# Kernel optimization log

Hardware: AMD Instinct MI355X
Metric: run time of the kernel (lower is better)

Reference implementation:

```python
import jax, jax.numpy as jnp
import numpy as np
from jax import lax

N, C_IN, C_OUT, W_DIM, RES = 16, 512, 512, 512, 64
K = 3                       # conv kernel (non-torgb)
UP, DOWN = 2, 2             # filtered_lrelu up/down factors
TAPS = 6 * UP               # 12-tap FIR filters (filter_size * factor)
FS = 128.0                  # tmp_sampling_rate = 2 * 64
CUTOFF, WIDTH = 8.0, 48.0   # cutoff Hz, transition width = 2*half_width
SLOPE, GAIN, CLAMP = 0.2, float(np.sqrt(2)), 256.0

# filtered_lrelu padding (StyleGAN3 formula); symmetric since square images
_pt = (RES - 1) * DOWN + 1 - (RES + K - 1) * UP + 2 * TAPS - 2
PX0 = PY0 = (_pt + UP) // 2   # = 9
PX1 = PY1 = _pt - PX0         # = 8


def design_lowpass_filter(numtaps, cutoff, width, fs):
    # scipy.signal.firwin with Kaiser window (width given), normalized to unit DC gain
    nyq = 0.5 * fs
    wn = width / nyq
    a = 2.285 * (numtaps - 1) * np.pi * wn + 7.95  # kaiser_atten
    if a > 50:
        beta = 0.1102 * (a - 8.7)
    elif a > 21:
        beta = 0.5842 * (a - 21) ** 0.4 + 0.07886 * (a - 21)
    else:
        beta = 0.0
    win = np.kaiser(numtaps, beta)
    m = np.arange(numtaps) - (numtaps - 1) / 2
    c = cutoff / nyq
    h = c * np.sinc(c * m) * win
    return (h / h.sum()).astype(np.float32)


def setup_inputs() -> dict:
    key = jax.random.key(0)
    ks = jax.random.split(key, 5)
    f = jnp.asarray(design_lowpass_filter(TAPS, CUTOFF, WIDTH, FS))
    return {
        "x": jax.random.normal(ks[0], (N, C_IN, RES, RES), jnp.float32),
        "w": jax.random.normal(ks[1], (N, W_DIM), jnp.float32),
        "affine_weight": jax.random.normal(ks[2], (C_IN, W_DIM), jnp.float32),
        "affine_bias": jnp.ones((C_IN,), jnp.float32),  # bias_init=1
        "conv_weight": jax.random.normal(ks[3], (C_OUT, C_IN, K, K), jnp.float32),
        "conv_bias": 0.1 * jax.random.normal(ks[4], (C_OUT,), jnp.float32),
        "up_filter": f,
        "down_filter": f,
    }


def _upfirdn2d_sep(x, f, up, down, pads, gain):
    # Separable upfirdn2d: zero-insert upsample, pad, FIR conv, strided downsample.
    # lhs_dilation gives (H-1)*up+1 samples; the up-1 trailing zeros of the torch
    # reference contribute nothing, so fold them into the high-side padding.
    px0, px1, py0, py1 = pads
    n, c, h, w = x.shape
    x = x.reshape(n * c, 1, h, w)
    x = lax.conv_general_dilated(x, f[None, None, :, None], (down, 1),
                                 [(py0, py1 + up - 1), (0, 0)], lhs_dilation=(up, 1),
                                 dimension_numbers=('NCHW', 'OIHW', 'NCHW'))
    x = lax.conv_general_dilated(x, f[None, None, None, :], (1, down),
                                 [(0, 0), (px0, px1 + up - 1)], lhs_dilation=(1, up),
                                 dimension_numbers=('NCHW', 'OIHW', 'NCHW'))
    return (x * gain).reshape(n, c, x.shape[2], x.shape[3])


def reference(x, w, affine_weight, affine_bias, conv_weight, conv_bias, up_filter, down_filter):
    # FullyConnectedLayer: weight_gain = 1/sqrt(w_dim)
    styles = w @ affine_weight.T * (1.0 / np.sqrt(W_DIM)) + affine_bias  # [N, C_IN]
    input_gain = 1.0  # magnitude_ema buffer == 1 -> rsqrt == 1

    # modulated_conv2d with demodulation (pre-normalize weight and styles)
    wt = conv_weight * lax.rsqrt(jnp.mean(conv_weight ** 2, axis=(1, 2, 3), keepdims=True))
    s = styles * lax.rsqrt(jnp.mean(styles ** 2))
    wk = wt[None] * s[:, None, :, None, None]             # [N, O, I, k, k]
    d = lax.rsqrt(jnp.sum(wk ** 2, axis=(2, 3, 4)) + 1e-8)  # [N, O]
    wk = wk * d[:, :, None, None, None] * input_gain

    def conv_one(xi, wi):  # xi [C,H,W], wi [O,I,k,k]; padding = kernel-1 = 2
        return lax.conv_general_dilated(xi[None], wi, (1, 1), [(K - 1, K - 1)] * 2,
                                        dimension_numbers=('NCHW', 'OIHW', 'NCHW'))[0]

    y = jax.vmap(conv_one)(x, wk)                         # [N, O, 66, 66]

    # filtered_lrelu: bias -> FIR upsample (gain=up^2) -> lrelu*sqrt(2)+clamp -> FIR downsample
    y = y + conv_bias[None, :, None, None]
    y = _upfirdn2d_sep(y, up_filter, UP, 1, (PX0, PX1, PY0, PY1), float(UP * UP))
    y = jnp.where(y >= 0, y, SLOPE * y) * GAIN
    y = jnp.clip(y, -CLAMP, CLAMP)
    y = _upfirdn2d_sep(y, down_filter, 1, DOWN, (0, 0, 0, 0), 1.0)
    return y  # [N, O, 64, 64]
```

## Files before the change

### kernel.cpp

```cpp
#include <hip/hip_runtime.h>
#include <hip/hip_bf16.h>

typedef __attribute__((ext_vector_type(8))) short bf16x8;
typedef __attribute__((ext_vector_type(4))) float f32x4;
typedef unsigned int u32;
typedef const __attribute__((address_space(1))) u32 glb_u32;
typedef __attribute__((address_space(3))) u32 lds_u32;

#define NB 16
#define CI 512
#define CO 512
#define PC 66
#define PADD 68
#define NCOLS (NB*PC*PC)

#define WS_STYLES 0ul
#define WS_SNORM  32768ul
#define WS_D      33024ul
#define WS_W2     65792ul
#define WS_AT     1114368ul
#define WS_XS     5832960ul
#define WS_CONV   81592576ul

__global__ void k_styles(const float* __restrict__ w, const float* __restrict__ aw,
                         const float* __restrict__ ab, float* __restrict__ styles) {
  int idx = blockIdx.x * 256 + threadIdx.x;
  int n = idx >> 9, i = idx & 511;
  const float* wr = w + n * 512;
  const float* ar = aw + i * 512;
  float s = 0.f;
  for (int j = 0; j < 512; ++j) s += wr[j] * ar[j];
  styles[idx] = s * 0.04419417382415922f + ab[i];
}

__global__ void k_snorm(const float* __restrict__ styles, float* __restrict__ snorm) {
  __shared__ float red[256];
  float s = 0.f;
  for (int e = threadIdx.x; e < 8192; e += 256) { float v = styles[e]; s += v * v; }
  red[threadIdx.x] = s;
  __syncthreads();
  for (int st = 128; st > 0; st >>= 1) {
    if (threadIdx.x < st) red[threadIdx.x] += red[threadIdx.x + st];
    __syncthreads();
  }
  if (threadIdx.x == 0) snorm[0] = rsqrtf(red[0] / 8192.f);
}

__global__ void k_wprep(const float* __restrict__ cw, __hip_bfloat16* __restrict__ At,
                        float* __restrict__ W2) {
  int o = blockIdx.x;
  const float* base = cw + o * 4608;
  __shared__ float red[256];
  __shared__ float wnorm_s;
  float s = 0.f;
  for (int e = threadIdx.x; e < 4608; e += 256) { float v = base[e]; s += v * v; }
  red[threadIdx.x] = s;
  __syncthreads();
  for (int st = 128; st > 0; st >>= 1) {
    if (threadIdx.x < st) red[threadIdx.x] += red[threadIdx.x + st];
    __syncthreads();
  }
  if (threadIdx.x == 0) wnorm_s = rsqrtf(red[0] / 4608.f);
  __syncthreads();
  float wn = wnorm_s;
  for (int i = threadIdx.x; i < 512; i += 256) {
    const float* e9 = cw + (o * 512 + i) * 9;
    float w2 = 0.f;
    int ic = i >> 5, ik = i & 31;
#pragma unroll
    for (int rs = 0; rs < 9; ++rs) {
      float wv = e9[rs] * wn;
      w2 += wv * wv;
      At[((ic * 9 + rs) * 512 + o) * 32 + ik] = __float2bfloat16(wv);
    }
    W2[o * 512 + i] = w2;
  }
}

__global__ void k_dcalc(const float* __restrict__ W2, const float* __restrict__ styles,
                        const float* __restrict__ snorm, float* __restrict__ d) {
  int idx = blockIdx.x * 256 + threadIdx.x;
  int n = idx >> 9, o = idx & 511;
  const float* w2r = W2 + o * 512;
  const float* sr = styles + n * 512;
  float sum = 0.f;
  for (int i = 0; i < 512; ++i) { float sv = sr[i]; sum += w2r[i] * sv * sv; }
  float sn = snorm[0];
  d[idx] = rsqrtf(sn * sn * sum + 1e-8f);
}

__global__ void k_zero_border(uint4* __restrict__ p) {
  int e = blockIdx.x * 256 + threadIdx.x;
  if (e >= 16 * 528 * 64) return;
  int chunk = e & 63;
  int rest = e >> 6;
  int n = rest / 528;
  int pos = rest - n * 528;
  int row, col;
  if (pos < 272) {
    int r = pos / 68;
    row = (r < 2) ? r : r + 64;
    col = pos - r * 68;
  } else {
    int q = pos - 272;
    row = 2 + (q >> 2);
    int cs = q & 3;
    col = (cs < 2) ? cs : cs + 64;
  }
  uint4 z = {0u, 0u, 0u, 0u};
  p[(n * 4624 + row * 68 + col) * 64 + chunk] = z;
}

__global__ void k_scale_tr(const float* __restrict__ x, const float* __restrict__ styles,
                           const float* __restrict__ snorm, __hip_bfloat16* __restrict__ xs) {
  const int i0 = blockIdx.x * 64;
  const int p = blockIdx.y;
  const int n = blockIdx.z;
  __shared__ float tile[64][65];
  const float sn = snorm[0];
  const int lo = threadIdx.x & 63;
  const int hi = threadIdx.x >> 6;
#pragma unroll 4
  for (int rep = 0; rep < 16; ++rep) {
    int ii = hi + rep * 4;
    float sc = styles[n * 512 + i0 + ii] * sn;
    tile[ii][lo] = x[((n * 512 + i0 + ii) * 64 + p) * 64 + lo] * sc;
  }
  __syncthreads();
  const int obase = (n * 4624 + (p + 2) * 68 + 2) * 512 + i0;
#pragma unroll 4
  for (int rep = 0; rep < 16; ++rep) {
    int q = hi + rep * 4;
    xs[obase + q * 512 + lo] = __float2bfloat16(tile[lo][q]);
  }
}

__device__ __forceinline__ int colbase_of(int c) {
  c = c < (NCOLS - 1) ? c : (NCOLS - 1);
  int n = (int)((unsigned)c / 4356u);
  int rem = c - n * 4356;
  int p = (int)((unsigned)rem / 66u);
  int q = rem - p * 66;
  return (n * 4624 + p * 68 + q) * 512;
}


#define GLD(G, L) __builtin_amdgcn_global_load_lds((glb_u32*)(G), (lds_u32*)(L), 16, 0, 0)
#define STAGE(KT2, KOFF2, CUR) do { \
    const char* _ga = AgA + (size_t)(KT2) * 32768; \
    char* _l = smem + (CUR) + sdst; \
    GLD(_ga, _l); \
    GLD(_ga + 4096, _l + 4096); \
    GLD(_ga + 8192, _l + 8192); \
    GLD(_ga + 12288, _l + 12288); \
    GLD(xsB0 + (KOFF2), _l + 16384); \
    GLD(xsB1 + (KOFF2), _l + 20480); } while (0)
#define BARR() __builtin_amdgcn_s_barrier()
#define LGKM() asm volatile("s_waitcnt lgkmcnt(0)" ::: "memory")
#define VMC6() asm volatile("s_waitcnt vmcnt(6)" ::: "memory")
#define VMC0() asm volatile("s_waitcnt vmcnt(0)" ::: "memory")

__global__ __launch_bounds__(256, 2) void k_gemm(
    const __hip_bfloat16* __restrict__ At, const __hip_bfloat16* __restrict__ xs,
    const float* __restrict__ dnorm, const float* __restrict__ cbias,
    __hip_bfloat16* __restrict__ cvt) {
  __shared__ __align__(16) char smem[49152];
  const int tid = threadIdx.x;

  const int bid = blockIdx.x;
  const int xcd = bid & 7, sidx = bid >> 3;
  const int wgid = (xcd < 2 ? xcd * 137 : 274 + (xcd - 2) * 136) + sidx;
  const int o0 = (wgid & 1) * 256;
  const int c0 = (wgid >> 1) * 128;

  const int lane = tid & 63, wave = tid >> 6;
  const int wr = wave >> 1, wc = wave & 1;
  const int r16 = lane & 15, sx = lane >> 4;
  const int poff = (r16 >> 1) * 128 + (((((r16 & 1) << 2) | sx)) ^ (r16 >> 1)) * 16;
  const int rdA = wr * 8192 + poff;
  const int rdB = 16384 + wc * 4096 + poff;

  const int p8 = (tid >> 3) & 7;
  const int s_log = (tid & 7) ^ p8;
  const int r0 = 2 * (tid >> 3) + (s_log >> 2);
  const int kc = s_log & 3;
  const int sdst = tid * 16;
  const char* AgA = (const char*)At + (size_t)(o0 + r0) * 64 + kc * 16;
  const char* xsC = (const char*)xs;
  const char* xsB0 = xsC + (size_t)(colbase_of(c0 + r0) * 2 + kc * 16);
  const char* xsB1 = xsC + (size_t)(colbase_of(c0 + 64 + r0) * 2 + kc * 16);

  f32x4 acc[8][4];
#pragma unroll
  for (int i = 0; i < 8; ++i)
#pragma unroll
    for (int j = 0; j < 4; ++j) acc[i][j] = (f32x4){0.f, 0.f, 0.f, 0.f};

  STAGE(0, 0, 0);
  STAGE(1, 1024, 24576);
  VMC6(); BARR();

  static const int OFF2[9] = {2048, 69632, 70656, 71680, 139264, 140288, 141312, 0, 1024};

  for (int ic = 0; ic < 16; ++ic) {
#pragma unroll
    for (int rs = 0; rs < 9; ++rs) {
      const int kt = ic * 9 + rs;
      const int curL = ((ic + rs) & 1) * 24576;
      bf16x8 af[8], bf[4];
#pragma unroll
      for (int m = 0; m < 8; ++m)
        af[m] = *(const bf16x8*)(smem + curL + rdA + m * 1024);
#pragma unroll
      for (int n = 0; n < 4; ++n)
        bf[n] = *(const bf16x8*)(smem + curL + rdB + n * 1024);
      LGKM();
      BARR();
      if (kt < 142) {
        const int koff2 = OFF2[rs] + (ic + (rs + 2) / 9) * 64;
        STAGE(kt + 2, koff2, curL);
      }
      __builtin_amdgcn_s_setprio(1);
#pragma unroll
      for (int m = 0; m < 8; ++m)
#pragma unroll
        for (int n = 0; n < 4; ++n)
          acc[m][n] = __builtin_amdgcn_mfma_f32_16x16x32_bf16(af[m], bf[n], acc[m][n], 0, 0, 0);
      __builtin_amdgcn_s_setprio(0);
      if (kt < 143) {
        if (kt < 142) VMC6(); else VMC0();
        BARR();
      }
    }
  }

  const int cb2 = c0 + wc * 64 + r16;
  const int rb = o0 + wr * 128 + (sx << 2);
#pragma unroll
  for (int nt = 0; nt < 4; ++nt) {
    int c = cb2 + nt * 16;
    if (c < NCOLS) {
      int n = (int)((unsigned)c / 4356u);
      int cadr = c + n * 2225916;
#pragma unroll
      for (int mt = 0; mt < 8; ++mt) {
#pragma unroll
        for (int reg = 0; reg < 4; ++reg) {
          int o = rb + mt * 16 + reg;
          float v = acc[mt][nt][reg] * dnorm[n * 512 + o] + cbias[o];
          cvt[cadr + o * 4356] = __float2bfloat16(v);
        }
      }
    }
  }
}

#define CSW 76
#define VSW 77
#define DHW 67
__global__ __launch_bounds__(512) void k_flrelu(
    const __hip_bfloat16* __restrict__ cvt, const float* __restrict__ fup,
    const float* __restrict__ fdn, float* __restrict__ out) {
  const int ch = blockIdx.x;
  const int n = blockIdx.y;
  const int tid = threadIdx.x;

  __shared__ float u_s[9246];
  __shared__ float vs_s[138 * VSW];

  const float fu0 = fup[0], fu1 = fup[1], fu2 = fup[2], fu3 = fup[3];
  const float fu4 = fup[4], fu5 = fup[5], fu6 = fup[6], fu7 = fup[7];
  const float fu8 = fup[8], fu9 = fup[9], fu10 = fup[10], fu11 = fup[11];
  const float fd0 = fdn[0], fd1 = fdn[1], fd2 = fdn[2], fd3 = fdn[3];
  const float fd4 = fdn[4], fd5 = fdn[5], fd6 = fdn[6], fd7 = fdn[7];
  const float fd8 = fdn[8], fd9 = fdn[9], fd10 = fdn[10], fd11 = fdn[11];

  const __hip_bfloat16* src = cvt + (size_t)(n * 512 + ch) * 4356;

  for (int e = tid; e < 75 * 75; e += 512) {
    int il = (int)((unsigned)e / 75u);
    int jl = e - il * 75;
    int i = il - 4, j = jl - 4;
    float v = 0.f;
    if (i >= 0 && i < 66 && j >= 0 && j < 66) v = __bfloat162float(src[i * 66 + j]);
    u_s[il * CSW + jl] = v;
  }
  __syncthreads();

  for (int e = tid; e < 69 * 75; e += 512) {
    int m = (int)((unsigned)e / 75u);
    int jl = e - m * 75;
    const float* col = u_s + jl;
    float c0 = col[(m + 0) * CSW], c1 = col[(m + 1) * CSW], c2 = col[(m + 2) * CSW];
    float c3 = col[(m + 3) * CSW], c4 = col[(m + 4) * CSW], c5 = col[(m + 5) * CSW];
    float ve = fu1 * c0 + fu3 * c1 + fu5 * c2 + fu7 * c3 + fu9 * c4 + fu11 * c5;
    float vo = fu0 * c0 + fu2 * c1 + fu4 * c2 + fu6 * c3 + fu8 * c4 + fu10 * c5;
    vs_s[(2 * m) * VSW + jl] = ve;
    vs_s[(2 * m + 1) * VSW + jl] = vo;
  }
  __syncthreads();

  if (tid < 276) {
    int h = (tid >= 138) ? 1 : 0;
    int fy = tid - h * 138;
    const float* vrow = vs_s + fy * VSW + 32 * h;
    float* dhrow = u_s + fy * DHW + 32 * h;
    float a0 = 0.f, a1 = 0.f, a2 = 0.f, a3 = 0.f, a4 = 0.f, a5 = 0.f;
    float w0 = vrow[0], w1 = vrow[1], w2 = vrow[2], w3 = vrow[3], w4 = vrow[4];
#pragma unroll
    for (int ql = 0; ql < 37; ++ql) {
      float w5 = vrow[ql + 5];
      float ge = fu1 * w0 + fu3 * w1 + fu5 * w2 + fu7 * w3 + fu9 * w4 + fu11 * w5;
      float go = fu0 * w0 + fu2 * w1 + fu4 * w2 + fu6 * w3 + fu8 * w4 + fu10 * w5;
      ge *= (ge >= 0.f) ? 5.656854249492381f : 1.1313708498984762f;
      go *= (go >= 0.f) ? 5.656854249492381f : 1.1313708498984762f;
      ge = fminf(fmaxf(ge, -256.f), 256.f);
      go = fminf(fmaxf(go, -256.f), 256.f);
      a0 += fd10 * ge + fd11 * go;
      a1 += fd8 * ge + fd9 * go;
      a2 += fd6 * ge + fd7 * go;
      a3 += fd4 * ge + fd5 * go;
      a4 += fd2 * ge + fd3 * go;
      a5 += fd0 * ge + fd1 * go;
      if (ql >= 5) dhrow[ql - 5] = a0;
      a0 = a1; a1 = a2; a2 = a3; a3 = a4; a4 = a5; a5 = 0.f;
      w0 = w1; w1 = w2; w2 = w3; w3 = w4; w4 = w5;
    }
  }
  __syncthreads();

  {
    int ox = tid & 63;
    int r = tid >> 6;
    const float* dcol = u_s + ox;
    int f0 = 16 * r;
    float wreg[12];
#pragma unroll
    for (int k = 0; k < 10; ++k) wreg[k] = dcol[(f0 + k) * DHW];
    float* dst = out + (((size_t)(n * 512 + ch) * 64 + 8 * r) * 64) + ox;
#pragma unroll
    for (int oyl = 0; oyl < 8; ++oyl) {
      wreg[10] = dcol[(f0 + 2 * oyl + 10) * DHW];
      wreg[11] = dcol[(f0 + 2 * oyl + 11) * DHW];
      float s = fd0 * wreg[0] + fd1 * wreg[1] + fd2 * wreg[2] + fd3 * wreg[3] +
                fd4 * wreg[4] + fd5 * wreg[5] + fd6 * wreg[6] + fd7 * wreg[7] +
                fd8 * wreg[8] + fd9 * wreg[9] + fd10 * wreg[10] + fd11 * wreg[11];
      dst[oyl * 64] = s;
#pragma unroll
      for (int k = 0; k < 10; ++k) wreg[k] = wreg[k + 2];
    }
  }
}

extern "C" void kernel_launch(void* const* d_in, const int* in_sizes, int n_in,
                              void* d_out, int out_size, void* d_ws, size_t ws_size,
                              hipStream_t stream) {
  const float* x = (const float*)d_in[0];
  const float* w = (const float*)d_in[1];
  const float* aw = (const float*)d_in[2];
  const float* ab = (const float*)d_in[3];
  const float* cw = (const float*)d_in[4];
  const float* cb = (const float*)d_in[5];
  const float* fu = (const float*)d_in[6];
  const float* fd = (const float*)d_in[7];
  char* ws = (char*)d_ws;
  float* styles = (float*)(ws + WS_STYLES);
  float* snorm = (float*)(ws + WS_SNORM);
  float* dmat = (float*)(ws + WS_D);
  float* W2 = (float*)(ws + WS_W2);
  __hip_bfloat16* At = (__hip_bfloat16*)(ws + WS_AT);
  __hip_bfloat16* xs = (__hip_bfloat16*)(ws + WS_XS);
  __hip_bfloat16* cvt = (__hip_bfloat16*)(ws + WS_CONV);
  float* out = (float*)d_out;

  k_styles<<<32, 256, 0, stream>>>(w, aw, ab, styles);
  k_snorm<<<1, 256, 0, stream>>>(styles, snorm);
  k_wprep<<<512, 256, 0, stream>>>(cw, At, W2);
  k_dcalc<<<32, 256, 0, stream>>>(W2, styles, snorm, dmat);
  k_zero_border<<<(16 * 528 * 64 + 255) / 256, 256, 0, stream>>>((uint4*)xs);
  k_scale_tr<<<dim3(8, 64, 16), 256, 0, stream>>>(x, styles, snorm, xs);
  k_gemm<<<1090, 256, 0, stream>>>(At, xs, dmat, cb, cvt);
  k_flrelu<<<dim3(512, 16), 512, 0, stream>>>(cvt, fu, fd, out);
}
```

Measured before the change: 814.0 us.

## Load GEMM A-operand directly into registers, keep only B in LDS ring

The conv GEMM no longer stages the weight (A) tile through LDS. Each wave reads its A fragments straight from global memory into two register sets that alternate, prefetched one k-step ahead. Only the activation (B) tile still goes through LDS, now as a 4-slot ring, which shrinks shared memory from 48KB to 32KB and removes the LGKM wait plus one barrier per k-step. Separately, the style and demod-coefficient kernels are vectorised to float4 loads. The cost is more vector registers and global-latency exposure on A, which is held together only by the hand-tuned vmcnt counts.

```diff
diff --git a/kernel.cpp b/kernel.cpp
--- a/kernel.cpp
+++ b/kernel.cpp
@@ -26,10 +26,13 @@
                          const float* __restrict__ ab, float* __restrict__ styles) {
   int idx = blockIdx.x * 256 + threadIdx.x;
   int n = idx >> 9, i = idx & 511;
-  const float* wr = w + n * 512;
-  const float* ar = aw + i * 512;
+  const float4* wr4 = (const float4*)(w + n * 512);
+  const float4* ar4 = (const float4*)(aw + i * 512);
   float s = 0.f;
-  for (int j = 0; j < 512; ++j) s += wr[j] * ar[j];
+  for (int j = 0; j < 128; ++j) {
+    float4 a = wr4[j], b = ar4[j];
+    s += a.x * b.x + a.y * b.y + a.z * b.z + a.w * b.w;
+  }
   styles[idx] = s * 0.04419417382415922f + ab[i];
 }
 
@@ -81,10 +84,13 @@
                         const float* __restrict__ snorm, float* __restrict__ d) {
   int idx = blockIdx.x * 256 + threadIdx.x;
   int n = idx >> 9, o = idx & 511;
-  const float* w2r = W2 + o * 512;
-  const float* sr = styles + n * 512;
+  const float4* w2r = (const float4*)(W2 + o * 512);
+  const float4* sr = (const float4*)(styles + n * 512);
   float sum = 0.f;
-  for (int i = 0; i < 512; ++i) { float sv = sr[i]; sum += w2r[i] * sv * sv; }
+  for (int i = 0; i < 128; ++i) {
+    float4 a = w2r[i], b = sr[i];
+    sum += a.x * b.x * b.x + a.y * b.y * b.y + a.z * b.z * b.z + a.w * b.w * b.w;
+  }
   float sn = snorm[0];
   d[idx] = rsqrtf(sn * sn * sum + 1e-8f);
 }
@@ -146,25 +152,46 @@
 
 
 #define GLD(G, L) __builtin_amdgcn_global_load_lds((glb_u32*)(G), (lds_u32*)(L), 16, 0, 0)
-#define STAGE(KT2, KOFF2, CUR) do { \
-    const char* _ga = AgA + (size_t)(KT2) * 32768; \
-    char* _l = smem + (CUR) + sdst; \
-    GLD(_ga, _l); \
-    GLD(_ga + 4096, _l + 4096); \
-    GLD(_ga + 8192, _l + 8192); \
-    GLD(_ga + 12288, _l + 12288); \
-    GLD(xsB0 + (KOFF2), _l + 16384); \
-    GLD(xsB1 + (KOFF2), _l + 20480); } while (0)
 #define BARR() __builtin_amdgcn_s_barrier()
-#define LGKM() asm volatile("s_waitcnt lgkmcnt(0)" ::: "memory")
-#define VMC6() asm volatile("s_waitcnt vmcnt(6)" ::: "memory")
-#define VMC0() asm volatile("s_waitcnt vmcnt(0)" ::: "memory")
+#define VMC10() asm volatile("s_waitcnt vmcnt(10)" ::: "memory")
+#define VMC8()  asm volatile("s_waitcnt vmcnt(8)" ::: "memory")
+#define VMC2()  asm volatile("s_waitcnt vmcnt(2)" ::: "memory")
+
+#define STAGEB(KT) do { \
+    int _kt = (KT); \
+    int _ic = (_kt * 456) >> 12; int _rs = _kt - 9 * _ic; \
+    int _ry = (_rs * 11) >> 5; int _rx = _rs - 3 * _ry; \
+    int _ko = _ry * 69632 + _rx * 1024 + _ic * 64; \
+    char* _l = smem + (_kt & 3) * 8192 + tid * 16; \
+    GLD(xsB0 + _ko, _l); \
+    GLD(xsB1 + _ko, _l + 4096); } while (0)
+
+#define STEP(T, CUR, NXT, DO_AF, DO_STAGE) do { \
+    const char* _bb = smem + ((T) & 3) * 8192 + rdB; \
+    bf16x8 _bf0 = *(const bf16x8*)(_bb); \
+    bf16x8 _bf1 = *(const bf16x8*)(_bb + 1024); \
+    bf16x8 _bf2 = *(const bf16x8*)(_bb + 2048); \
+    bf16x8 _bf3 = *(const bf16x8*)(_bb + 3072); \
+    if (DO_AF) { \
+      const char* _ap = ApC + (size_t)((T) + 1) * 32768; \
+      _Pragma("unroll") for (int _m = 0; _m < 8; ++_m) \
+        NXT[_m] = *(const bf16x8*)(_ap + _m * 1024); \
+    } \
+    if (DO_STAGE) STAGEB((T) + 2); \
+    __builtin_amdgcn_s_setprio(1); \
+    _Pragma("unroll") for (int _m = 0; _m < 8; ++_m) { \
+      acc[_m][0] = __builtin_amdgcn_mfma_f32_16x16x32_bf16(CUR[_m], _bf0, acc[_m][0], 0, 0, 0); \
+      acc[_m][1] = __builtin_amdgcn_mfma_f32_16x16x32_bf16(CUR[_m], _bf1, acc[_m][1], 0, 0, 0); \
+      acc[_m][2] = __builtin_amdgcn_mfma_f32_16x16x32_bf16(CUR[_m], _bf2, acc[_m][2], 0, 0, 0); \
+      acc[_m][3] = __builtin_amdgcn_mfma_f32_16x16x32_bf16(CUR[_m], _bf3, acc[_m][3], 0, 0, 0); \
+    } \
+    __builtin_amdgcn_s_setprio(0); } while (0)
 
 __global__ __launch_bounds__(256, 2) void k_gemm(
     const __hip_bfloat16* __restrict__ At, const __hip_bfloat16* __restrict__ xs,
     const float* __restrict__ dnorm, const float* __restrict__ cbias,
     __hip_bfloat16* __restrict__ cvt) {
-  __shared__ __align__(16) char smem[49152];
+  __shared__ __align__(16) char smem[32768];
   const int tid = threadIdx.x;
 
   const int bid = blockIdx.x;
@@ -177,62 +204,42 @@
   const int wr = wave >> 1, wc = wave & 1;
   const int r16 = lane & 15, sx = lane >> 4;
   const int poff = (r16 >> 1) * 128 + (((((r16 & 1) << 2) | sx)) ^ (r16 >> 1)) * 16;
-  const int rdA = wr * 8192 + poff;
-  const int rdB = 16384 + wc * 4096 + poff;
+  const int rdB = wc * 4096 + poff;
 
   const int p8 = (tid >> 3) & 7;
   const int s_log = (tid & 7) ^ p8;
   const int r0 = 2 * (tid >> 3) + (s_log >> 2);
   const int kc = s_log & 3;
-  const int sdst = tid * 16;
-  const char* AgA = (const char*)At + (size_t)(o0 + r0) * 64 + kc * 16;
   const char* xsC = (const char*)xs;
   const char* xsB0 = xsC + (size_t)(colbase_of(c0 + r0) * 2 + kc * 16);
   const char* xsB1 = xsC + (size_t)(colbase_of(c0 + 64 + r0) * 2 + kc * 16);
 
+  const char* ApC = (const char*)(At + (size_t)(o0 + wr * 128 + r16) * 32 + sx * 8);
+
   f32x4 acc[8][4];
 #pragma unroll
   for (int i = 0; i < 8; ++i)
 #pragma unroll
     for (int j = 0; j < 4; ++j) acc[i][j] = (f32x4){0.f, 0.f, 0.f, 0.f};
-
-  STAGE(0, 0, 0);
-  STAGE(1, 1024, 24576);
-  VMC6(); BARR();
-
-  static const int OFF2[9] = {2048, 69632, 70656, 71680, 139264, 140288, 141312, 0, 1024};
-
-  for (int ic = 0; ic < 16; ++ic) {
-#pragma unroll
-    for (int rs = 0; rs < 9; ++rs) {
-      const int kt = ic * 9 + rs;
-      const int curL = ((ic + rs) & 1) * 24576;
-      bf16x8 af[8], bf[4];
-#pragma unroll
-      for (int m = 0; m < 8; ++m)
-        af[m] = *(const bf16x8*)(smem + curL + rdA + m * 1024);
-#pragma unroll
-      for (int n = 0; n < 4; ++n)
-        bf[n] = *(const bf16x8*)(smem + curL + rdB + n * 1024);
-      LGKM();
-      BARR();
-      if (kt < 142) {
-        const int koff2 = OFF2[rs] + (ic + (rs + 2) / 9) * 64;
-        STAGE(kt + 2, koff2, curL);
-      }
-      __builtin_amdgcn_s_setprio(1);
-#pragma unroll
-      for (int m = 0; m < 8; ++m)
-#pragma unroll
-        for (int n = 0; n < 4; ++n)
-          acc[m][n] = __builtin_amdgcn_mfma_f32_16x16x32_bf16(af[m], bf[n], acc[m][n], 0, 0, 0);
-      __builtin_amdgcn_s_setprio(0);
-      if (kt < 143) {
-        if (kt < 142) VMC6(); else VMC0();
-        BARR();
-      }
-    }
-  }
+  bf16x8 afA[8], afB[8];
+
+#pragma unroll
+  for (int m = 0; m < 8; ++m)
+    afA[m] = *(const bf16x8*)(ApC + m * 1024);
+  STAGEB(0);
+  STAGEB(1);
+  VMC2(); BARR();
+
+  for (int kp = 0; kp < 71; ++kp) {
+    const int t0 = 2 * kp;
+    STEP(t0, afA, afB, 1, 1);
+    VMC10(); BARR();
+    STEP(t0 + 1, afB, afA, 1, 1);
+    VMC10(); BARR();
+  }
+  STEP(142, afA, afB, 1, 0);
+  VMC8(); BARR();
+  STEP(143, afB, afA, 0, 0);
 
   const int cb2 = c0 + wc * 64 + r16;
   const int rb = o0 + wr * 128 + (sx << 2);
```

Result: slower. 964.5 us (+18.5%).
